# Optimization experiments

Hardware: AMD Instinct MI355X
Metric: run time of the kernel (lower is better)

Reference implementation:

```python
import jax, jax.numpy as jnp
import numpy as np

D_MODEL = 1024
NUM_HEADS = 16
HEAD_DIM = D_MODEL // NUM_HEADS
THETA = 10000.0


def _init_linear(key, d_out, d_in):
    sigma = np.sqrt(2.0 / (d_in + d_out))
    w = jax.random.truncated_normal(key, -3.0, 3.0, (d_out, d_in), dtype=jnp.float32)
    return w * sigma


def setup_inputs() -> dict:
    key = jax.random.key(0)
    kh, kq, kk, kv, ko = jax.random.split(key, 5)
    h = jax.random.normal(kh, (2, 2048, D_MODEL), dtype=jnp.float32)
    return {
        "h": h,
        "wq": _init_linear(kq, D_MODEL, D_MODEL),
        "wk": _init_linear(kk, D_MODEL, D_MODEL),
        "wv": _init_linear(kv, D_MODEL, D_MODEL),
        "wo": _init_linear(ko, D_MODEL, D_MODEL),
    }


def _rope(x, pos):
    # x: [B, H, T, dh]; rotate interleaved pairs (..., 2k, 2k+1)
    dh = x.shape[-1]
    freq = THETA ** (-jnp.arange(0, dh // 2, dtype=jnp.float32) / (dh // 2))
    ang = pos[:, None] * freq[None, :]            # [T, dh/2]
    cos, sin = jnp.cos(ang), jnp.sin(ang)
    xr = x.reshape(*x.shape[:-1], dh // 2, 2)
    x0, x1 = xr[..., 0], xr[..., 1]
    out = jnp.stack((cos * x0 - sin * x1, sin * x0 + cos * x1), axis=-1)
    return out.reshape(x.shape)


def reference(h, wq, wk, wv, wo):
    B, T, D = h.shape
    Hn, dh = NUM_HEADS, HEAD_DIM

    def split_heads(x):  # [B,T,D] -> [B,H,T,dh]
        return x.reshape(B, T, Hn, dh).transpose(0, 2, 1, 3)

    Q = split_heads(h @ wq.T)
    K = split_heads(h @ wk.T)
    V = split_heads(h @ wv.T)

    pos = jnp.arange(T, dtype=jnp.float32)
    Q = _rope(Q, pos)
    K = _rope(K, pos)

    scores = jnp.einsum('bhqd,bhkd->bhqk', Q, K) / jnp.sqrt(jnp.float32(dh))
    mask = jnp.tril(jnp.ones((T, T), dtype=bool))
    scores = jnp.where(mask, scores, -jnp.inf)
    attn = jax.nn.softmax(scores, axis=-1)
    out = jnp.einsum('bhqk,bhkd->bhqd', attn, V)   # [B,H,T,dh]
    out = out.transpose(0, 2, 1, 3).reshape(B, T, D)
    return out @ wo.T
```

## Files before the change

### kernel.cpp

```cpp
#include <hip/hip_runtime.h>
#include <math.h>

typedef __bf16 bf16_t;
typedef __bf16 v8bf __attribute__((ext_vector_type(8)));
typedef __bf16 v4bf __attribute__((ext_vector_type(4)));
typedef float  v4f  __attribute__((ext_vector_type(4)));

#define AS1 __attribute__((address_space(1)))
#define AS3 __attribute__((address_space(3)))

static __device__ __forceinline__ void load_lds16(const bf16_t* g, bf16_t* l) {
    __builtin_amdgcn_global_load_lds((AS1 void*)const_cast<bf16_t*>(g),
                                     (AS3 void*)l, 16, 0, 0);
}
static __device__ __forceinline__ void load_lds16b(const char* g, char* l) {
    __builtin_amdgcn_global_load_lds((AS1 void*)const_cast<char*>(g),
                                     (AS3 void*)l, 16, 0, 0);
}

static __device__ __forceinline__ void fast_sincos(float ang, float* sn, float* cs) {
    float rv = ang * 0.15915494309189535f;
    rv -= floorf(rv);
    const float a = rv * 6.283185307179586f;
    *sn = __sinf(a);
    *cs = __cosf(a);
}

__global__ __launch_bounds__(256) void cvt_fp32_bf16(
    const float* __restrict__ h,  const float* __restrict__ wq,
    const float* __restrict__ wk, const float* __restrict__ wv,
    const float* __restrict__ wo,
    bf16_t* __restrict__ hb,  bf16_t* __restrict__ wqb,
    bf16_t* __restrict__ wkb, bf16_t* __restrict__ wvb,
    bf16_t* __restrict__ wob)
{
    const size_t HM = (size_t)4 << 20;
    const size_t i8 = ((size_t)blockIdx.x * 256 + threadIdx.x) * 8;
    const float* src; bf16_t* dst; size_t off;
    if (i8 < HM) { src = h; dst = hb; off = i8; }
    else {
        const size_t r = (i8 - HM) >> 20;
        off = (i8 - HM) & (((size_t)1 << 20) - 1);
        src = (r == 0) ? wq  : (r == 1) ? wk  : (r == 2) ? wv  : wo;
        dst = (r == 0) ? wqb : (r == 1) ? wkb : (r == 2) ? wvb : wob;
    }
    const float4 a = *(const float4*)(src + off);
    const float4 b = *(const float4*)(src + off + 4);
    v8bf o;
    o[0]=(bf16_t)a.x; o[1]=(bf16_t)a.y; o[2]=(bf16_t)a.z; o[3]=(bf16_t)a.w;
    o[4]=(bf16_t)b.x; o[5]=(bf16_t)b.y; o[6]=(bf16_t)b.z; o[7]=(bf16_t)b.w;
    *(v8bf*)(dst + off) = o;
}

__global__ __launch_bounds__(256) void qkv_gemm_rope(
    const bf16_t* __restrict__ A,
    const bf16_t* __restrict__ wq,
    const bf16_t* __restrict__ wk,
    const bf16_t* __restrict__ wv,
    bf16_t* __restrict__ qo, bf16_t* __restrict__ ko, bf16_t* __restrict__ vo)
{
    __shared__ __align__(16) bf16_t smem[17408];
    bf16_t* As = smem;
    bf16_t* Bs = smem + 4096;

    const int tid = threadIdx.x;
    const int n0  = blockIdx.x * 128;
    const int m0  = blockIdx.y * 128;
    const int sel = n0 >> 10;
    const bf16_t* W = (sel == 0) ? wq : (sel == 1) ? wk : wv;
    const int wr0 = n0 & 1023;

    const int wave = tid >> 6;
    const int lane = tid & 63;
    const int l16  = lane & 15;
    const int quad = lane >> 4;
    const int wrow = (wave >> 1) * 64;
    const int wcol = (wave & 1) * 64;

    v4f acc[4][4];
    #pragma unroll
    for (int i = 0; i < 4; ++i)
        #pragma unroll
        for (int j = 0; j < 4; ++j) acc[i][j] = (v4f)(0.0f);

    for (int kt = 0; kt < 32; ++kt) {
        const int k0 = kt * 32;
        #pragma unroll
        for (int rep = 0; rep < 2; ++rep) {
            const int c   = rep * 256 + tid;
            const int row = c >> 2;
            const int col = (c & 3) * 8;
            load_lds16(A + (size_t)(m0 + row) * 1024 + k0 + col, &As[c * 8]);
            load_lds16(W + (size_t)(wr0 + row) * 1024 + k0 + col, &Bs[c * 8]);
        }
        __syncthreads();

        v8bf af[4], bfb[4];
        #pragma unroll
        for (int i = 0; i < 4; ++i) {
            af[i]  = *(const v8bf*)&As[(wrow + i * 16 + l16) * 32 + quad * 8];
            bfb[i] = *(const v8bf*)&Bs[(wcol + i * 16 + l16) * 32 + quad * 8];
        }
        #pragma unroll
        for (int i = 0; i < 4; ++i)
            #pragma unroll
            for (int j = 0; j < 4; ++j)
                acc[i][j] = __builtin_amdgcn_mfma_f32_16x16x32_bf16(
                    af[i], bfb[j], acc[i][j], 0, 0, 0);
        __syncthreads();
    }

    bf16_t* Ls = smem + wave * 4352;
    const int bq     = (m0 + wrow) >> 11;
    const int hd     = ((n0 + wcol) >> 6) & 15;
    const int t_base = (m0 + wrow) & 2047;

    if (sel < 2) {
        bf16_t* OUT = (sel == 0) ? qo : ko;
        #pragma unroll
        for (int i = 0; i < 4; ++i) {
            #pragma unroll
            for (int j = 0; j < 4; ++j) {
                #pragma unroll
                for (int r = 0; r < 4; ++r) {
                    const int mrow = i * 16 + quad * 4 + r;
                    const int dcol = j * 16 + l16;
                    float v = acc[i][j][r];
                    const float vp = __shfl_xor(v, 1);
                    const int t  = t_base + mrow;
                    const int kk = dcol >> 1;
                    const float freq = exp2f((float)kk * -0.4152410118609203f);
                    float sn, cs;
                    fast_sincos((float)t * freq, &sn, &cs);
                    v = ((dcol & 1) == 0) ? (cs * v - sn * vp) : (sn * vp + cs * v);
                    Ls[mrow * 68 + dcol] = (bf16_t)v;
                }
            }
        }
        #pragma unroll
        for (int s = 0; s < 8; ++s) {
            const int row = s * 8 + (lane >> 3);
            const int off = (lane & 7) * 8;
            const v8bf vv = *(const v8bf*)&Ls[row * 68 + off];
            *(v8bf*)(OUT + (((size_t)(bq * 16 + hd) * 2048) + t_base + row) * 64 + off) = vv;
        }
    } else {
        #pragma unroll
        for (int i = 0; i < 4; ++i)
            #pragma unroll
            for (int j = 0; j < 4; ++j) {
                v4bf p;
                #pragma unroll
                for (int r = 0; r < 4; ++r) p[r] = (bf16_t)acc[i][j][r];
                *(v4bf*)&Ls[(j * 16 + l16) * 68 + i * 16 + quad * 4] = p;
            }
        #pragma unroll
        for (int s = 0; s < 8; ++s) {
            const int drow = s * 8 + (lane >> 3);
            const int off  = (lane & 7) * 8;
            const v8bf vv = *(const v8bf*)&Ls[drow * 68 + off];
            *(v8bf*)(vo + (((size_t)(bq * 16 + hd) * 64) + drow) * 2048 + t_base + off) = vv;
        }
    }
}

__global__ __launch_bounds__(256, 4) void attn_mfma(
    const bf16_t* __restrict__ qg,
    const bf16_t* __restrict__ kg,
    const bf16_t* __restrict__ vtg,
    bf16_t* __restrict__ og)
{
    __shared__ __align__(16) bf16_t Ks[2][4096];
    __shared__ __align__(16) bf16_t Vs[2][4096];
    __shared__ __align__(16) bf16_t Ps[4][1024];

    const int tid  = threadIdx.x;
    const int wave = tid >> 6;
    const int lane = tid & 63;
    const int l16  = lane & 15;
    const int quad = lane >> 4;

    const int i   = blockIdx.x;
    const int xcd = i & 7;
    const int j   = i >> 3;
    const int bhl = j >> 5;
    const int u   = j & 31;
    const int q64 = (bhl & 1) ? (31 - u) : u;
    const int bh  = xcd * 4 + bhl;
    const int b = bh >> 4, hh = bh & 15;

    const char* Kb = (const char*)(kg  + (size_t)bh * 2048 * 64);
    const char* Vb = (const char*)(vtg + (size_t)bh * 64 * 2048);

    const int qglb = q64 * 64 + wave * 16 + l16;

    const int sw  = (l16 & 7) << 4;
    const int cb0 = (quad << 4) ^ sw;

    const int grow = tid >> 3;
    const int gsw  = ((tid & 7) << 4) ^ ((grow & 7) << 4);

    const bf16_t* qrow = qg + ((size_t)bh * 2048 + qglb) * 64;
    v8bf qf[2];
    qf[0] = *(const v8bf*)(qrow + quad * 8);
    qf[1] = *(const v8bf*)(qrow + 32 + quad * 8);
    #pragma unroll
    for (int e = 0; e < 8; ++e) {
        qf[0][e] = (bf16_t)((float)qf[0][e] * 0.18033688011112042f);
        qf[1][e] = (bf16_t)((float)qf[1][e] * 0.18033688011112042f);
    }

    v8bf ones1;
    #pragma unroll
    for (int e = 0; e < 8; ++e) ones1[e] = (bf16_t)1.0f;

    float m_r = -1e30f;
    v4f l_acc = (v4f)(0.0f);
    v4f o_acc[4];
    #pragma unroll
    for (int d = 0; d < 4; ++d) o_acc[d] = (v4f)(0.0f);

    {
        const char* ks = Kb + ((size_t)grow << 7) + gsw;
        const char* vs = Vb + ((size_t)grow << 12) + gsw;
        char* kd = (char*)Ks[0] + tid * 16;
        char* vd = (char*)Vs[0] + tid * 16;
        load_lds16b(ks, kd);
        load_lds16b(ks + (32 << 7), kd + 4096);
        load_lds16b(vs, vd);
        load_lds16b(vs + ((size_t)32 << 12), vd + 4096);
    }

    for (int kt = 0; kt <= q64; ++kt) {
        const int cur = kt & 1;
        const int nxt = cur ^ 1;
        __syncthreads();

        if (kt < q64) {
            const char* ks = Kb + ((size_t)((kt + 1) * 64 + grow) << 7) + gsw;
            const char* vs = Vb + ((size_t)grow << 12) + ((size_t)(kt + 1) << 7) + gsw;
            char* kd = (char*)Ks[nxt] + tid * 16;
            char* vd = (char*)Vs[nxt] + tid * 16;
            load_lds16b(ks, kd);
            load_lds16b(ks + (32 << 7), kd + 4096);
            load_lds16b(vs, vd);
            load_lds16b(vs + ((size_t)32 << 12), vd + 4096);
        }

        const char* ksc = (const char*)Ks[cur];
        v4f s_acc[4];
        #pragma unroll
        for (int kblk = 0; kblk < 4; ++kblk) s_acc[kblk] = (v4f)(0.0f);
        #pragma unroll
        for (int kblk = 0; kblk < 4; ++kblk) {
            const char* kr = ksc + ((kblk * 16 + l16) << 7);
            const v8bf kf0 = *(const v8bf*)(kr + cb0);
            const v8bf kf1 = *(const v8bf*)(kr + (cb0 ^ 64));
            s_acc[kblk] = __builtin_amdgcn_mfma_f32_16x16x32_bf16(
                kf0, qf[0], s_acc[kblk], 0, 0, 0);
            s_acc[kblk] = __builtin_amdgcn_mfma_f32_16x16x32_bf16(
                kf1, qf[1], s_acc[kblk], 0, 0, 0);
        }

        if (kt == q64) {
            #pragma unroll
            for (int kblk = 0; kblk < 4; ++kblk)
                #pragma unroll
                for (int r = 0; r < 4; ++r)
                    if (kt * 64 + kblk * 16 + quad * 4 + r > qglb)
                        s_acc[kblk][r] = -1e30f;
        }

        float mx = -1e30f;
        #pragma unroll
        for (int kblk = 0; kblk < 4; ++kblk)
            #pragma unroll
            for (int r = 0; r < 4; ++r) mx = fmaxf(mx, s_acc[kblk][r]);
        mx = fmaxf(mx, __shfl_xor(mx, 16));
        mx = fmaxf(mx, __shfl_xor(mx, 32));
        if (!__all(mx - m_r <= 8.0f)) {
            const float mn = fmaxf(m_r, mx);
            const float a  = exp2f(m_r - mn);
            m_r = mn;
            l_acc *= a;
            #pragma unroll
            for (int d = 0; d < 4; ++d) o_acc[d] *= a;
        }

        char* psc = (char*)Ps[wave] + (l16 << 7);
        #pragma unroll
        for (int kblk = 0; kblk < 4; ++kblk) {
            v4bf p;
            #pragma unroll
            for (int r = 0; r < 4; ++r)
                p[r] = (bf16_t)exp2f(s_acc[kblk][r] - m_r);
            *(v4bf*)(psc + ((kblk * 32 + quad * 8) ^ sw)) = p;
        }
        const v8bf pf0 = *(const v8bf*)(psc + cb0);
        const v8bf pf1 = *(const v8bf*)(psc + (cb0 ^ 64));

        const char* vsc = (const char*)Vs[cur];
        #pragma unroll
        for (int dblk = 0; dblk < 4; ++dblk) {
            const char* vr = vsc + ((dblk * 16 + l16) << 7);
            const v8bf vf0 = *(const v8bf*)(vr + cb0);
            const v8bf vf1 = *(const v8bf*)(vr + (cb0 ^ 64));
            o_acc[dblk] = __builtin_amdgcn_mfma_f32_16x16x32_bf16(
                vf0, pf0, o_acc[dblk], 0, 0, 0);
            o_acc[dblk] = __builtin_amdgcn_mfma_f32_16x16x32_bf16(
                vf1, pf1, o_acc[dblk], 0, 0, 0);
        }
        l_acc = __builtin_amdgcn_mfma_f32_16x16x32_bf16(ones1, pf0, l_acc, 0, 0, 0);
        l_acc = __builtin_amdgcn_mfma_f32_16x16x32_bf16(ones1, pf1, l_acc, 0, 0, 0);
    }

    const float inv_l = 1.0f / l_acc[0];
    const size_t base = ((size_t)b * 2048 + qglb) * 1024 + hh * 64;
    #pragma unroll
    for (int dblk = 0; dblk < 4; ++dblk) {
        v4bf o;
        #pragma unroll
        for (int r = 0; r < 4; ++r) o[r] = (bf16_t)(o_acc[dblk][r] * inv_l);
        *(v4bf*)(og + base + dblk * 16 + quad * 4) = o;
    }
}

__global__ __launch_bounds__(256) void out_gemm(
    const bf16_t* __restrict__ A,
    const bf16_t* __restrict__ W,
    float* __restrict__ C)
{
    __shared__ __align__(16) float smemf[4352];
    bf16_t* As = (bf16_t*)smemf;
    bf16_t* Bs = As + 4096;

    const int tid = threadIdx.x;
    const int n0  = blockIdx.x * 64;
    const int m0  = blockIdx.y * 128;

    const int wave = tid >> 6;
    const int lane = tid & 63;
    const int l16  = lane & 15;
    const int quad = lane >> 4;
    const int wrow = (wave >> 1) * 64;
    const int wcol = (wave & 1) * 32;

    v4f acc[4][2];
    #pragma unroll
    for (int i = 0; i < 4; ++i)
        #pragma unroll
        for (int j = 0; j < 2; ++j) acc[i][j] = (v4f)(0.0f);

    for (int kt = 0; kt < 32; ++kt) {
        const int k0 = kt * 32;
        #pragma unroll
        for (int rep = 0; rep < 2; ++rep) {
            const int c   = rep * 256 + tid;
            const int row = c >> 2;
            const int col = (c & 3) * 8;
            load_lds16(A + (size_t)(m0 + row) * 1024 + k0 + col, &As[c * 8]);
        }
        {
            const int row = tid >> 2;
            const int col = (tid & 3) * 8;
            load_lds16(W + (size_t)(n0 + row) * 1024 + k0 + col, &Bs[tid * 8]);
        }
        __syncthreads();

        v8bf af[4], bfb[2];
        #pragma unroll
        for (int i = 0; i < 4; ++i)
            af[i]  = *(const v8bf*)&As[(wrow + i * 16 + l16) * 32 + quad * 8];
        #pragma unroll
        for (int j = 0; j < 2; ++j)
            bfb[j] = *(const v8bf*)&Bs[(wcol + j * 16 + l16) * 32 + quad * 8];
        #pragma unroll
        for (int i = 0; i < 4; ++i)
            #pragma unroll
            for (int j = 0; j < 2; ++j)
                acc[i][j] = __builtin_amdgcn_mfma_f32_16x16x32_bf16(
                    af[i], bfb[j], acc[i][j], 0, 0, 0);
        __syncthreads();
    }

    float* Lw = smemf + wave * 1088;
    #pragma unroll
    for (int half = 0; half < 2; ++half) {
        #pragma unroll
        for (int ii = 0; ii < 2; ++ii) {
            const int i = half * 2 + ii;
            #pragma unroll
            for (int j = 0; j < 2; ++j)
                #pragma unroll
                for (int r = 0; r < 4; ++r)
                    Lw[(ii * 16 + quad * 4 + r) * 34 + j * 16 + l16] = acc[i][j][r];
        }
        #pragma unroll
        for (int s = 0; s < 8; ++s) {
            const int row = s * 4 + (lane >> 4);
            const float2 vv = *(const float2*)&Lw[row * 34 + l16 * 2];
            *(float2*)(C + (size_t)(m0 + wrow + half * 32 + row) * 1024
                         + n0 + wcol + l16 * 2) = vv;
        }
    }
}

extern "C" void kernel_launch(void* const* d_in, const int* in_sizes, int n_in,
                              void* d_out, int out_size, void* d_ws, size_t ws_size,
                              hipStream_t stream) {
    const float* h  = (const float*)d_in[0];
    const float* wq = (const float*)d_in[1];
    const float* wk = (const float*)d_in[2];
    const float* wv = (const float*)d_in[3];
    const float* wo = (const float*)d_in[4];

    const size_t NH = (size_t)4096 * 1024;
    const size_t NW = (size_t)1024 * 1024;

    bf16_t* hb  = (bf16_t*)d_ws;
    bf16_t* wqb = hb  + NH;
    bf16_t* wkb = wqb + NW;
    bf16_t* wvb = wkb + NW;
    bf16_t* wob = wvb + NW;
    bf16_t* qw  = wob + NW;
    bf16_t* kw  = qw + NH;
    bf16_t* vw  = kw + NH;
    bf16_t* og  = hb;

    cvt_fp32_bf16<<<dim3(4096), dim3(256), 0, stream>>>(
        h, wq, wk, wv, wo, hb, wqb, wkb, wvb, wob);
    qkv_gemm_rope<<<dim3(24, 32), dim3(256), 0, stream>>>(
        hb, wqb, wkb, wvb, qw, kw, vw);
    attn_mfma<<<dim3(1024), dim3(256), 0, stream>>>(qw, kw, vw, og);
    out_gemm<<<dim3(16, 32), dim3(256), 0, stream>>>(og, wob, (float*)d_out);
}
```

Measured before the change: 187.9 us.

## Double-buffer LDS tiles in projection GEMMs and use RoPE angle recurrence

The QKV and output projection GEMMs now use two LDS buffers. The next k-tile's global-to-LDS loads are issued right after the barrier, so they overlap with the MFMAs on the current tile, and one barrier per iteration is removed. The RoPE epilogue no longer evaluates exp2 and sincos for every element: it computes a base angle per column once and steps cos/sin forward with angle-addition rotations. This raises LDS use in the output GEMM and can add small rounding drift to the rotated values.

```diff
diff --git a/kernel.cpp b/kernel.cpp
--- a/kernel.cpp
+++ b/kernel.cpp
@@ -60,8 +60,6 @@
     bf16_t* __restrict__ qo, bf16_t* __restrict__ ko, bf16_t* __restrict__ vo)
 {
     __shared__ __align__(16) bf16_t smem[17408];
-    bf16_t* As = smem;
-    bf16_t* Bs = smem + 4096;
 
     const int tid = threadIdx.x;
     const int n0  = blockIdx.x * 128;
@@ -83,18 +81,29 @@
         #pragma unroll
         for (int j = 0; j < 4; ++j) acc[i][j] = (v4f)(0.0f);
 
+    const int c0r  = tid >> 2;
+    const int c0c  = (tid & 3) * 8;
+    #define QKV_STAGE(bbuf, ktile)                                             \
+        {                                                                      \
+            const int k0_ = (ktile) * 32;                                      \
+            load_lds16(A + (size_t)(m0 + c0r) * 1024 + k0_ + c0c,              \
+                       smem + (bbuf) * 4096 + tid * 8);                        \
+            load_lds16(A + (size_t)(m0 + 64 + c0r) * 1024 + k0_ + c0c,         \
+                       smem + (bbuf) * 4096 + 2048 + tid * 8);                 \
+            load_lds16(W + (size_t)(wr0 + c0r) * 1024 + k0_ + c0c,             \
+                       smem + 8192 + (bbuf) * 4096 + tid * 8);                 \
+            load_lds16(W + (size_t)(wr0 + 64 + c0r) * 1024 + k0_ + c0c,        \
+                       smem + 8192 + (bbuf) * 4096 + 2048 + tid * 8);          \
+        }
+
+    QKV_STAGE(0, 0);
     for (int kt = 0; kt < 32; ++kt) {
-        const int k0 = kt * 32;
-        #pragma unroll
-        for (int rep = 0; rep < 2; ++rep) {
-            const int c   = rep * 256 + tid;
-            const int row = c >> 2;
-            const int col = (c & 3) * 8;
-            load_lds16(A + (size_t)(m0 + row) * 1024 + k0 + col, &As[c * 8]);
-            load_lds16(W + (size_t)(wr0 + row) * 1024 + k0 + col, &Bs[c * 8]);
-        }
+        const int cur = kt & 1;
         __syncthreads();
-
+        if (kt < 31) QKV_STAGE(cur ^ 1, kt + 1);
+
+        const bf16_t* As = smem + cur * 4096;
+        const bf16_t* Bs = smem + 8192 + cur * 4096;
         v8bf af[4], bfb[4];
         #pragma unroll
         for (int i = 0; i < 4; ++i) {
@@ -107,8 +116,9 @@
             for (int j = 0; j < 4; ++j)
                 acc[i][j] = __builtin_amdgcn_mfma_f32_16x16x32_bf16(
                     af[i], bfb[j], acc[i][j], 0, 0, 0);
-        __syncthreads();
-    }
+    }
+    __syncthreads();
+    #undef QKV_STAGE
 
     bf16_t* Ls = smem + wave * 4352;
     const int bq     = (m0 + wrow) >> 11;
@@ -118,22 +128,36 @@
     if (sel < 2) {
         bf16_t* OUT = (sel == 0) ? qo : ko;
         #pragma unroll
-        for (int i = 0; i < 4; ++i) {
-            #pragma unroll
-            for (int j = 0; j < 4; ++j) {
+        for (int j = 0; j < 4; ++j) {
+            const int dcol = j * 16 + l16;
+            const int kk   = dcol >> 1;
+            const float f  = exp2f((float)kk * -0.4152410118609203f);
+            float cb, sb, c1, s1, c16, s16;
+            fast_sincos((float)(t_base + quad * 4) * f, &sb, &cb);
+            fast_sincos(f, &s1, &c1);
+            fast_sincos(16.0f * f, &s16, &c16);
+            float ci = cb, si = sb;
+            #pragma unroll
+            for (int i = 0; i < 4; ++i) {
+                float cr = ci, sr = si;
                 #pragma unroll
                 for (int r = 0; r < 4; ++r) {
                     const int mrow = i * 16 + quad * 4 + r;
-                    const int dcol = j * 16 + l16;
                     float v = acc[i][j][r];
                     const float vp = __shfl_xor(v, 1);
-                    const int t  = t_base + mrow;
-                    const int kk = dcol >> 1;
-                    const float freq = exp2f((float)kk * -0.4152410118609203f);
-                    float sn, cs;
-                    fast_sincos((float)t * freq, &sn, &cs);
-                    v = ((dcol & 1) == 0) ? (cs * v - sn * vp) : (sn * vp + cs * v);
+                    v = ((dcol & 1) == 0) ? (cr * v - sr * vp)
+                                          : (sr * vp + cr * v);
                     Ls[mrow * 68 + dcol] = (bf16_t)v;
+                    if (r < 3) {
+                        const float cn = cr * c1 - sr * s1;
+                        sr = sr * c1 + cr * s1;
+                        cr = cn;
+                    }
+                }
+                if (i < 3) {
+                    const float cn = ci * c16 - si * s16;
+                    si = si * c16 + ci * s16;
+                    ci = cn;
                 }
             }
         }
@@ -330,9 +354,8 @@
     const bf16_t* __restrict__ W,
     float* __restrict__ C)
 {
-    __shared__ __align__(16) float smemf[4352];
-    bf16_t* As = (bf16_t*)smemf;
-    bf16_t* Bs = As + 4096;
+    __shared__ __align__(16) float smemf[6144];
+    bf16_t* Sb = (bf16_t*)smemf;
 
     const int tid = threadIdx.x;
     const int n0  = blockIdx.x * 64;
@@ -351,22 +374,27 @@
         #pragma unroll
         for (int j = 0; j < 2; ++j) acc[i][j] = (v4f)(0.0f);
 
+    const int c0r = tid >> 2;
+    const int c0c = (tid & 3) * 8;
+    #define OUT_STAGE(bbuf, ktile)                                             \
+        {                                                                      \
+            const int k0_ = (ktile) * 32;                                      \
+            load_lds16(A + (size_t)(m0 + c0r) * 1024 + k0_ + c0c,              \
+                       Sb + (bbuf) * 4096 + tid * 8);                          \
+            load_lds16(A + (size_t)(m0 + 64 + c0r) * 1024 + k0_ + c0c,         \
+                       Sb + (bbuf) * 4096 + 2048 + tid * 8);                   \
+            load_lds16(W + (size_t)(n0 + (tid >> 2)) * 1024 + k0_ + c0c,       \
+                       Sb + 8192 + (bbuf) * 2048 + tid * 8);                   \
+        }
+
+    OUT_STAGE(0, 0);
     for (int kt = 0; kt < 32; ++kt) {
-        const int k0 = kt * 32;
-        #pragma unroll
-        for (int rep = 0; rep < 2; ++rep) {
-            const int c   = rep * 256 + tid;
-            const int row = c >> 2;
-            const int col = (c & 3) * 8;
-            load_lds16(A + (size_t)(m0 + row) * 1024 + k0 + col, &As[c * 8]);
-        }
-        {
-            const int row = tid >> 2;
-            const int col = (tid & 3) * 8;
-            load_lds16(W + (size_t)(n0 + row) * 1024 + k0 + col, &Bs[tid * 8]);
-        }
+        const int cur = kt & 1;
         __syncthreads();
-
+        if (kt < 31) OUT_STAGE(cur ^ 1, kt + 1);
+
+        const bf16_t* As = Sb + cur * 4096;
+        const bf16_t* Bs = Sb + 8192 + cur * 2048;
         v8bf af[4], bfb[2];
         #pragma unroll
         for (int i = 0; i < 4; ++i)
@@ -380,8 +408,9 @@
             for (int j = 0; j < 2; ++j)
                 acc[i][j] = __builtin_amdgcn_mfma_f32_16x16x32_bf16(
                     af[i], bfb[j], acc[i][j], 0, 0, 0);
-        __syncthreads();
-    }
+    }
+    __syncthreads();
+    #undef OUT_STAGE
 
     float* Lw = smemf + wave * 1088;
     #pragma unroll
```

Result: no change. 186.6 us (-0.7%).
